# Optimization experiments

Measured on AMD Instinct MI355X. Metric: run time of the kernel, lower is better.

The kernel has to match this reference:

```python
import jax, jax.numpy as jnp
import numpy as np

B, T, C = 4, 4096, 1024
H = 16
D = C // H
EPS = 1e-06


def setup_inputs() -> dict:
    key = jax.random.key(0)
    k1, k2, k3 = jax.random.split(key, 3)
    x = jax.random.normal(k1, (B, T, C), dtype=jnp.float32)
    Wqkv = jax.random.normal(k2, (3 * C, C), dtype=jnp.float32) * (1.0 / np.sqrt(C))
    Wproj = jax.random.normal(k3, (C, C), dtype=jnp.float32) * (1.0 / np.sqrt(C))
    bproj = jnp.zeros((C,), dtype=jnp.float32)
    return {"x": x, "Wqkv": Wqkv, "Wproj": Wproj, "bproj": bproj}


def _phi(x):
    # elu(x) + 1 kernel feature map (non-negative)
    return jax.nn.elu(x) + 1.0


def reference(x, Wqkv, Wproj, bproj):
    b, t, c = x.shape
    qkv = jnp.einsum('btc,ec->bte', x, Wqkv)              # (B,T,3C)
    qkv = qkv.reshape(b, t, 3, H, D)
    q, k, v = qkv[:, :, 0], qkv[:, :, 1], qkv[:, :, 2]     # (B,T,H,D)
    q = _phi(q)
    k = _phi(k)
    # kv state: sum over sequence of outer products k_d v_m -> (B,H,D,D)
    kv = jnp.einsum('bnhd,bnhm->bhdm', k, v)
    k_sum = k.sum(axis=1)                                  # (B,H,D)
    out = jnp.einsum('bnhd,bhdm->bnhm', q, kv)             # (B,T,H,D)
    normalizer = jnp.einsum('bnhd,bhd->bnh', q, k_sum) + EPS
    out = out / normalizer[..., None]
    out = out.reshape(b, t, c)
    out = jnp.einsum('btc,oc->bto', out, Wproj) + bproj
    return out
```

## Files before the change

kernel.cpp:

```cpp
#include <hip/hip_runtime.h>

typedef __bf16 bf16;
typedef bf16 bf16x8 __attribute__((ext_vector_type(8)));
typedef bf16 bf16x4 __attribute__((ext_vector_type(4)));
typedef float f32x4 __attribute__((ext_vector_type(4)));

#define B_ 4
#define T_ 4096
#define C_ 1024
#define EPS_ 1e-6f
#define KVTSTR 16448

typedef __attribute__((address_space(1))) const void* as1p;
typedef __attribute__((address_space(3))) void* as3p;

__global__ void cast_all(const float* __restrict__ x, const float* __restrict__ wq,
                         const float* __restrict__ wp, bf16* __restrict__ xw,
                         bf16* __restrict__ wqw, bf16* __restrict__ wpw) {
  const int N0 = 16777216 / 8, N1 = 3145728 / 8, N2 = 1048576 / 8;
  int i = blockIdx.x * blockDim.x + threadIdx.x;
  const int stride = gridDim.x * blockDim.x;
  for (; i < N0 + N1 + N2; i += stride) {
    const float* src;
    bf16* dst;
    int j;
    if (i < N0) { src = x; dst = xw; j = i; }
    else if (i < N0 + N1) { src = wq; dst = wqw; j = i - N0; }
    else { src = wp; dst = wpw; j = i - N0 - N1; }
    const float4* p = (const float4*)(src + (size_t)j * 8);
    float4 v0 = p[0];
    float4 v1 = p[1];
    bf16x8 o;
    o[0] = (bf16)v0.x; o[1] = (bf16)v0.y; o[2] = (bf16)v0.z; o[3] = (bf16)v0.w;
    o[4] = (bf16)v1.x; o[5] = (bf16)v1.y; o[6] = (bf16)v1.z; o[7] = (bf16)v1.w;
    *(bf16x8*)(dst + (size_t)j * 8) = o;
  }
}

#define BM 256
#define BN 256
#define BK 64
#define KD 1024
#define NTI (KD / BK)
#define TILB 32768
#define BUFB (2 * TILB)
#define SMEMB (2 * BUFB)

#define STG(p, ko, dst) __builtin_amdgcn_global_load_lds((as1p)((p) + (ko)), (as3p)(dst), 16, 0, 0)

#define LDA(MI0)                                                                       \
  _Pragma("unroll") for (int a = 0; a < 2; a++)                                        \
    _Pragma("unroll") for (int kk = 0; kk < 2; kk++)                                   \
      af[a][kk] = *(const bf16x8*)(Ab + (wm * 128 + ((MI0) + a) * 16 + fr) * 64 + swz[kk]);

#define MM(MI0)                                                                        \
  __builtin_amdgcn_s_setprio(1);                                                       \
  _Pragma("unroll") for (int a = 0; a < 2; a++)                                        \
    _Pragma("unroll") for (int nj = 0; nj < 4; nj++)                                   \
      _Pragma("unroll") for (int kk = 0; kk < 2; kk++)                                 \
        acc[(MI0) + a][nj] = __builtin_amdgcn_mfma_f32_16x16x32_bf16(af[a][kk], bfr[nj][kk], acc[(MI0) + a][nj], 0, 0, 0); \
  __builtin_amdgcn_s_setprio(0);

#define BAR1 { __builtin_amdgcn_s_barrier(); asm volatile("s_waitcnt lgkmcnt(0)" ::: "memory"); __builtin_amdgcn_sched_barrier(0); }
#define BAR2 { __builtin_amdgcn_s_barrier(); __builtin_amdgcn_sched_barrier(0); }

template <int MODE>
__global__ __launch_bounds__(512, 1) void gemmX(
    const bf16* __restrict__ A, const bf16* __restrict__ Bm,
    void* __restrict__ Cout, const float* __restrict__ bias,
    bf16* __restrict__ kvt, int M, int N, int tiles_n) {
  extern __shared__ char smem[];
  const int tid = threadIdx.x;
  const int l = tid & 63;
  const int w = tid >> 6;
  const int wm = w >> 2;
  const int wn = w & 3;

  const int cpx = gridDim.x >> 3;
  const int bid = (blockIdx.x & 7) * cpx + (blockIdx.x >> 3);
  const int tm = (bid / tiles_n) * BM;
  const int tn = (bid % tiles_n) * BN;

  const int gsw = ((tid & 7) ^ ((tid >> 3) & 7)) * 8;
  const int tsr = tid >> 3;

  const bf16* pA0 = A + (size_t)(tm + tsr) * KD + gsw;
  const bf16* pA1 = A + (size_t)(tm + 64 + tsr) * KD + gsw;
  const bf16* pA2 = A + (size_t)(tm + 128 + tsr) * KD + gsw;
  const bf16* pA3 = A + (size_t)(tm + 192 + tsr) * KD + gsw;
  const bf16* pB0 = Bm + (size_t)(tn + tsr) * KD + gsw;
  const bf16* pB1 = Bm + (size_t)(tn + 64 + tsr) * KD + gsw;
  const bf16* pB2 = Bm + (size_t)(tn + 128 + tsr) * KD + gsw;
  const bf16* pB3 = Bm + (size_t)(tn + 192 + tsr) * KD + gsw;

  const int fr = l & 15;
  const int fc = l >> 4;
  int swz[2];
  swz[0] = ((0 * 4 + fc) ^ (fr & 7)) * 8;
  swz[1] = ((1 * 4 + fc) ^ (fr & 7)) * 8;

  f32x4 acc[8][4] = {};

  STG(pB0, 0, smem + TILB + tid * 16);
  STG(pB1, 0, smem + TILB + 8192 + tid * 16);
  STG(pB2, 0, smem + TILB + 16384 + tid * 16);
  STG(pB3, 0, smem + TILB + 24576 + tid * 16);
  STG(pA0, 0, smem + tid * 16);
  STG(pA2, 0, smem + 16384 + tid * 16);
  STG(pA1, 0, smem + 8192 + tid * 16);
  STG(pA3, 0, smem + 24576 + tid * 16);
  asm volatile("s_waitcnt vmcnt(2)" ::: "memory");
  __builtin_amdgcn_s_barrier();
  __builtin_amdgcn_sched_barrier(0);

  for (int t = 0; t < NTI; ++t) {
    const bf16* Ab = (const bf16*)(smem + (t & 1) * BUFB);
    const bf16* Bb = (const bf16*)(smem + (t & 1) * BUFB + TILB);
    char* sd = smem + ((t & 1) ^ 1) * BUFB;
    const bool st = (t + 1 < NTI);
    const int ko = (t + 1) * BK;
    bf16x8 bfr[4][2], af[2][2];

#pragma unroll
    for (int nj = 0; nj < 4; nj++)
#pragma unroll
      for (int kk = 0; kk < 2; kk++)
        bfr[nj][kk] = *(const bf16x8*)(Bb + (wn * 64 + nj * 16 + fr) * 64 + swz[kk]);
    LDA(0)
    if (st) {
      STG(pB0, ko, sd + TILB + tid * 16);
      STG(pB1, ko, sd + TILB + 8192 + tid * 16);
      STG(pB2, ko, sd + TILB + 16384 + tid * 16);
      STG(pB3, ko, sd + TILB + 24576 + tid * 16);
    }
    BAR1 MM(0) BAR2

    LDA(2)
    if (st) {
      STG(pA0, ko, sd + tid * 16);
      STG(pA2, ko, sd + 16384 + tid * 16);
      STG(pA1, ko, sd + 8192 + tid * 16);
      STG(pA3, ko, sd + 24576 + tid * 16);
    }
    BAR1 MM(2)
    if (st) { asm volatile("s_waitcnt vmcnt(8)" ::: "memory"); }
    else    { asm volatile("s_waitcnt vmcnt(0)" ::: "memory"); }
    BAR2

    LDA(4)
    BAR1 MM(4) BAR2

    LDA(6)
    BAR1 MM(6)
    if (st) { asm volatile("s_waitcnt vmcnt(2)" ::: "memory"); }
    BAR2
  }

  const int crow0 = tm + wm * 128 + (l >> 4) * 4;
  const int ccol0 = tn + wn * 64 + (l & 15);
  if (MODE == 0) {
    if (tn < 1024) {
      bf16* qbuf = (bf16*)Cout;
#pragma unroll
      for (int mi = 0; mi < 8; mi++)
#pragma unroll
        for (int nj = 0; nj < 4; nj++) {
          const int col = ccol0 + nj * 16;
#pragma unroll
          for (int r = 0; r < 4; r++) {
            const int row = crow0 + mi * 16 + r;
            float v = acc[mi][nj][r];
            v = (v > 0.f) ? (v + 1.0f) : __expf(v);
            qbuf[(size_t)row * 1024 + col] = (bf16)v;
          }
        }
    } else {
#pragma unroll
      for (int mi = 0; mi < 8; mi++)
#pragma unroll
        for (int nj = 0; nj < 4; nj++) {
          const int colp = ccol0 + nj * 16 - 1024;
          const bool isk = (colp < 1024);
          bf16x4 pk;
#pragma unroll
          for (int r = 0; r < 4; r++) {
            float v = acc[mi][nj][r];
            if (isk) v = (v > 0.f) ? (v + 1.0f) : __expf(v);
            pk[r] = (bf16)v;
          }
          const int n0 = crow0 + mi * 16;
          *(bf16x4*)(kvt + (size_t)colp * KVTSTR + n0) = pk;
        }
    }
  } else {
    float* Cf = (float*)Cout;
#pragma unroll
    for (int mi = 0; mi < 8; mi++)
#pragma unroll
      for (int nj = 0; nj < 4; nj++) {
        const int col = ccol0 + nj * 16;
        const float bv = bias[col];
#pragma unroll
        for (int r = 0; r < 4; r++) {
          const int row = crow0 + mi * 16 + r;
          Cf[(size_t)row * N + col] = acc[mi][nj][r] + bv;
        }
      }
  }
}

__global__ __launch_bounds__(256) void kvgemm(const bf16* __restrict__ kvt,
                                              float* __restrict__ partial) {
  const int kc = blockIdx.x >> 6;
  const int bh = blockIdx.x & 63;
  const int b = bh >> 4, h = bh & 15;
  const int l = threadIdx.x & 63;
  const int w = threadIdx.x >> 6;

  const size_t nb = (size_t)b * 4096 + kc * 1024 + (l >> 4) * 8;
  const bf16* Ar = kvt + (size_t)(h * 64 + w * 16 + (l & 15)) * KVTSTR + nb;
  const bf16* Br = kvt + (size_t)(1024 + h * 64 + (l & 15)) * KVTSTR + nb;

  f32x4 acc[4] = {};
  float ks = 0.f;
  bf16x8 aC, bC[4], aN, bN[4];
  aC = *(const bf16x8*)Ar;
#pragma unroll
  for (int nj = 0; nj < 4; nj++) bC[nj] = *(const bf16x8*)(Br + (size_t)nj * 16 * KVTSTR);

  for (int it = 0; it < 32; ++it) {
    if (it + 1 < 32) {
      aN = *(const bf16x8*)(Ar + (it + 1) * 32);
#pragma unroll
      for (int nj = 0; nj < 4; nj++)
        bN[nj] = *(const bf16x8*)(Br + (size_t)nj * 16 * KVTSTR + (it + 1) * 32);
    }
#pragma unroll
    for (int i = 0; i < 8; i++) ks += (float)aC[i];
#pragma unroll
    for (int nj = 0; nj < 4; nj++)
      acc[nj] = __builtin_amdgcn_mfma_f32_16x16x32_bf16(aC, bC[nj], acc[nj], 0, 0, 0);
    aC = aN;
#pragma unroll
    for (int nj = 0; nj < 4; nj++) bC[nj] = bN[nj];
  }

  ks += __shfl_xor(ks, 16);
  ks += __shfl_xor(ks, 32);

  float* p = partial + (size_t)(kc * 64 + bh) * 4160;
#pragma unroll
  for (int nj = 0; nj < 4; nj++) {
    const int m = nj * 16 + (l & 15);
#pragma unroll
    for (int r = 0; r < 4; r++) {
      const int d = w * 16 + (l >> 4) * 4 + r;
      p[d * 64 + m] = acc[nj][r];
    }
  }
  if (l < 16) p[4096 + w * 16 + l] = ks;
}

__global__ void kv_finalize(const float* __restrict__ partial, bf16* __restrict__ kvb) {
  const int bh = blockIdx.x;
  for (int i = threadIdx.x; i < 80 * 64; i += 256) {
    const int row = i >> 6;
    const int dd = i & 63;
    float outv = 0.f;
    if (row < 64) {
      float s = 0.f;
#pragma unroll
      for (int kc = 0; kc < 4; kc++)
        s += partial[(size_t)(kc * 64 + bh) * 4160 + dd * 64 + row];
      outv = s;
    } else if (row < 66) {
      float s = 0.f;
#pragma unroll
      for (int kc = 0; kc < 4; kc++)
        s += partial[(size_t)(kc * 64 + bh) * 4160 + 4096 + dd];
      bf16 hi = (bf16)s;
      outv = (row == 64) ? (float)hi : (s - (float)hi);
    }
    kvb[(size_t)bh * 5120 + row * 64 + dd] = (bf16)outv;
  }
}

__global__ __launch_bounds__(256) void attn_mfma(const bf16* __restrict__ qbuf,
                                                 const bf16* __restrict__ kvb,
                                                 bf16* __restrict__ attn) {
  const int bh = blockIdx.x >> 4;
  const int tch = blockIdx.x & 15;
  const int b = bh >> 4;
  const int h = bh & 15;
  const int lane = threadIdx.x & 63;
  const int wave = threadIdx.x >> 6;
  const int t0 = tch * 256 + wave * 64;

  const bf16* kvp = kvb + (size_t)bh * 5120;
  bf16x8 bfrag[5][2];
#pragma unroll
  for (int j = 0; j < 5; j++)
#pragma unroll
    for (int kk = 0; kk < 2; kk++)
      bfrag[j][kk] = *(const bf16x8*)(kvp + (j * 16 + (lane & 15)) * 64 + kk * 32 + (lane >> 4) * 8);

  f32x4 acc[4][5] = {};
#pragma unroll
  for (int i = 0; i < 4; i++) {
    const int t = t0 + i * 16 + (lane & 15);
    const bf16* qp = qbuf + (size_t)(b * T_ + t) * 1024 + h * 64 + (lane >> 4) * 8;
    bf16x8 a0 = *(const bf16x8*)qp;
    bf16x8 a1 = *(const bf16x8*)(qp + 32);
#pragma unroll
    for (int j = 0; j < 5; j++) {
      acc[i][j] = __builtin_amdgcn_mfma_f32_16x16x32_bf16(a0, bfrag[j][0], acc[i][j], 0, 0, 0);
      acc[i][j] = __builtin_amdgcn_mfma_f32_16x16x32_bf16(a1, bfrag[j][1], acc[i][j], 0, 0, 0);
    }
  }

#pragma unroll
  for (int i = 0; i < 4; i++) {
#pragma unroll
    for (int r = 0; r < 4; r++) {
      float hi = __shfl(acc[i][4][r], (lane & 48));
      float lo = __shfl(acc[i][4][r], (lane & 48) + 1);
      float inv = 1.0f / (hi + lo + EPS_);
      const int t = t0 + i * 16 + (lane >> 4) * 4 + r;
      bf16* op = attn + (size_t)(b * T_ + t) * 1024 + h * 64 + (lane & 15);
#pragma unroll
      for (int j = 0; j < 4; j++)
        op[j * 16] = (bf16)(acc[i][j][r] * inv);
    }
  }
}

extern "C" void kernel_launch(void* const* d_in, const int* in_sizes, int n_in,
                              void* d_out, int out_size, void* d_ws, size_t ws_size,
                              hipStream_t stream) {
  const float* x = (const float*)d_in[0];
  const float* Wqkv = (const float*)d_in[1];
  const float* Wproj = (const float*)d_in[2];
  const float* bproj = (const float*)d_in[3];
  float* out = (float*)d_out;

  char* w = (char*)d_ws;
  bf16* xw = (bf16*)w;      w += (size_t)16777216 * 2;
  bf16* wqkv = (bf16*)w;    w += (size_t)3145728 * 2;
  bf16* wproj = (bf16*)w;   w += (size_t)1048576 * 2;
  bf16* qbuf = (bf16*)w;    w += (size_t)16384 * 1024 * 2;
  bf16* kvt = (bf16*)w;     w += (size_t)2048 * KVTSTR * 2;
  bf16* attnb = (bf16*)w;   w += (size_t)16384 * 1024 * 2;
  float* partial = (float*)w; w += (size_t)4 * 64 * 4160 * 4;
  bf16* kvb = (bf16*)w;

  (void)hipFuncSetAttribute((const void*)gemmX<0>,
      hipFuncAttributeMaxDynamicSharedMemorySize, SMEMB);
  (void)hipFuncSetAttribute((const void*)gemmX<1>,
      hipFuncAttributeMaxDynamicSharedMemorySize, SMEMB);

  cast_all<<<2048, 256, 0, stream>>>(x, Wqkv, Wproj, xw, wqkv, wproj);

  gemmX<0><<<768, 512, SMEMB, stream>>>(xw, wqkv, (void*)qbuf, nullptr, kvt, 16384, 3072, 12);

  kvgemm<<<256, 256, 0, stream>>>(kvt, partial);
  kv_finalize<<<64, 256, 0, stream>>>(partial, kvb);

  attn_mfma<<<64 * 16, 256, 0, stream>>>(qbuf, kvb, attnb);

  gemmX<1><<<256, 512, SMEMB, stream>>>(attnb, wproj, (void*)out, bproj, nullptr, 16384, 1024, 4);
}
```

Before: 221.1 us.

## Replace 256x256 GEMM tiles with 128x256 BK32 tiles and higher occupancy

New measurement: 236.6 us. 1.07x slower.

```diff
diff --git a/kernel.cpp b/kernel.cpp
--- a/kernel.cpp
+++ b/kernel.cpp
@@ -37,39 +37,23 @@
   }
 }
 
-#define BM 256
+#define BM 128
 #define BN 256
-#define BK 64
+#define BK 32
 #define KD 1024
 #define NTI (KD / BK)
-#define TILB 32768
-#define BUFB (2 * TILB)
-#define SMEMB (2 * BUFB)
+#define ABY 8192
+#define BBY 16384
+#define BUFBY (ABY + BBY)
 
 #define STG(p, ko, dst) __builtin_amdgcn_global_load_lds((as1p)((p) + (ko)), (as3p)(dst), 16, 0, 0)
 
-#define LDA(MI0)                                                                       \
-  _Pragma("unroll") for (int a = 0; a < 2; a++)                                        \
-    _Pragma("unroll") for (int kk = 0; kk < 2; kk++)                                   \
-      af[a][kk] = *(const bf16x8*)(Ab + (wm * 128 + ((MI0) + a) * 16 + fr) * 64 + swz[kk]);
-
-#define MM(MI0)                                                                        \
-  __builtin_amdgcn_s_setprio(1);                                                       \
-  _Pragma("unroll") for (int a = 0; a < 2; a++)                                        \
-    _Pragma("unroll") for (int nj = 0; nj < 4; nj++)                                   \
-      _Pragma("unroll") for (int kk = 0; kk < 2; kk++)                                 \
-        acc[(MI0) + a][nj] = __builtin_amdgcn_mfma_f32_16x16x32_bf16(af[a][kk], bfr[nj][kk], acc[(MI0) + a][nj], 0, 0, 0); \
-  __builtin_amdgcn_s_setprio(0);
-
-#define BAR1 { __builtin_amdgcn_s_barrier(); asm volatile("s_waitcnt lgkmcnt(0)" ::: "memory"); __builtin_amdgcn_sched_barrier(0); }
-#define BAR2 { __builtin_amdgcn_s_barrier(); __builtin_amdgcn_sched_barrier(0); }
-
 template <int MODE>
-__global__ __launch_bounds__(512, 1) void gemmX(
+__global__ __launch_bounds__(512, 4) void gemmT(
     const bf16* __restrict__ A, const bf16* __restrict__ Bm,
     void* __restrict__ Cout, const float* __restrict__ bias,
     bf16* __restrict__ kvt, int M, int N, int tiles_n) {
-  extern __shared__ char smem[];
+  __shared__ char smem[2 * BUFBY];
   const int tid = threadIdx.x;
   const int l = tid & 63;
   const int w = tid >> 6;
@@ -81,88 +65,66 @@
   const int tm = (bid / tiles_n) * BM;
   const int tn = (bid % tiles_n) * BN;
 
-  const int gsw = ((tid & 7) ^ ((tid >> 3) & 7)) * 8;
-  const int tsr = tid >> 3;
+  const int gsw = ((tid & 3) ^ ((tid >> 3) & 3)) * 8;
+  const int tsr = tid >> 2;
 
   const bf16* pA0 = A + (size_t)(tm + tsr) * KD + gsw;
-  const bf16* pA1 = A + (size_t)(tm + 64 + tsr) * KD + gsw;
-  const bf16* pA2 = A + (size_t)(tm + 128 + tsr) * KD + gsw;
-  const bf16* pA3 = A + (size_t)(tm + 192 + tsr) * KD + gsw;
   const bf16* pB0 = Bm + (size_t)(tn + tsr) * KD + gsw;
-  const bf16* pB1 = Bm + (size_t)(tn + 64 + tsr) * KD + gsw;
-  const bf16* pB2 = Bm + (size_t)(tn + 128 + tsr) * KD + gsw;
-  const bf16* pB3 = Bm + (size_t)(tn + 192 + tsr) * KD + gsw;
+  const bf16* pB1 = Bm + (size_t)(tn + 128 + tsr) * KD + gsw;
 
   const int fr = l & 15;
   const int fc = l >> 4;
-  int swz[2];
-  swz[0] = ((0 * 4 + fc) ^ (fr & 7)) * 8;
-  swz[1] = ((1 * 4 + fc) ^ (fr & 7)) * 8;
-
-  f32x4 acc[8][4] = {};
-
-  STG(pB0, 0, smem + TILB + tid * 16);
-  STG(pB1, 0, smem + TILB + 8192 + tid * 16);
-  STG(pB2, 0, smem + TILB + 16384 + tid * 16);
-  STG(pB3, 0, smem + TILB + 24576 + tid * 16);
+  const int fsw = (fc ^ ((fr >> 1) & 3)) * 8;
+
+  f32x4 acc[4][4] = {};
+
   STG(pA0, 0, smem + tid * 16);
-  STG(pA2, 0, smem + 16384 + tid * 16);
-  STG(pA1, 0, smem + 8192 + tid * 16);
-  STG(pA3, 0, smem + 24576 + tid * 16);
-  asm volatile("s_waitcnt vmcnt(2)" ::: "memory");
+  STG(pB0, 0, smem + ABY + tid * 16);
+  STG(pB1, 0, smem + ABY + 8192 + tid * 16);
+  asm volatile("s_waitcnt vmcnt(0)" ::: "memory");
   __builtin_amdgcn_s_barrier();
   __builtin_amdgcn_sched_barrier(0);
 
+#pragma unroll 2
   for (int t = 0; t < NTI; ++t) {
-    const bf16* Ab = (const bf16*)(smem + (t & 1) * BUFB);
-    const bf16* Bb = (const bf16*)(smem + (t & 1) * BUFB + TILB);
-    char* sd = smem + ((t & 1) ^ 1) * BUFB;
-    const bool st = (t + 1 < NTI);
-    const int ko = (t + 1) * BK;
-    bf16x8 bfr[4][2], af[2][2];
-
+    char* rb = smem + (t & 1) * BUFBY;
+    char* sd = smem + ((t & 1) ^ 1) * BUFBY;
+    if (t + 1 < NTI) {
+      const int ko = (t + 1) * BK;
+      STG(pA0, ko, sd + tid * 16);
+      STG(pB0, ko, sd + ABY + tid * 16);
+      STG(pB1, ko, sd + ABY + 8192 + tid * 16);
+    }
+    const bf16* Ab = (const bf16*)rb;
+    const bf16* Bb = (const bf16*)(rb + ABY);
+    bf16x8 af[4], bfr[4];
+#pragma unroll
+    for (int mi = 0; mi < 4; mi++)
+      af[mi] = *(const bf16x8*)(Ab + (wm * 64 + mi * 16 + fr) * 32 + fsw);
 #pragma unroll
     for (int nj = 0; nj < 4; nj++)
-#pragma unroll
-      for (int kk = 0; kk < 2; kk++)
-        bfr[nj][kk] = *(const bf16x8*)(Bb + (wn * 64 + nj * 16 + fr) * 64 + swz[kk]);
-    LDA(0)
-    if (st) {
-      STG(pB0, ko, sd + TILB + tid * 16);
-      STG(pB1, ko, sd + TILB + 8192 + tid * 16);
-      STG(pB2, ko, sd + TILB + 16384 + tid * 16);
-      STG(pB3, ko, sd + TILB + 24576 + tid * 16);
-    }
-    BAR1 MM(0) BAR2
-
-    LDA(2)
-    if (st) {
-      STG(pA0, ko, sd + tid * 16);
-      STG(pA2, ko, sd + 16384 + tid * 16);
-      STG(pA1, ko, sd + 8192 + tid * 16);
-      STG(pA3, ko, sd + 24576 + tid * 16);
-    }
-    BAR1 MM(2)
-    if (st) { asm volatile("s_waitcnt vmcnt(8)" ::: "memory"); }
-    else    { asm volatile("s_waitcnt vmcnt(0)" ::: "memory"); }
-    BAR2
-
-    LDA(4)
-    BAR1 MM(4) BAR2
-
-    LDA(6)
-    BAR1 MM(6)
-    if (st) { asm volatile("s_waitcnt vmcnt(2)" ::: "memory"); }
-    BAR2
-  }
-
-  const int crow0 = tm + wm * 128 + (l >> 4) * 4;
+      bfr[nj] = *(const bf16x8*)(Bb + (wn * 64 + nj * 16 + fr) * 32 + fsw);
+    asm volatile("s_waitcnt lgkmcnt(0)" ::: "memory");
+    __builtin_amdgcn_sched_barrier(0);
+    __builtin_amdgcn_s_setprio(1);
+#pragma unroll
+    for (int mi = 0; mi < 4; mi++)
+#pragma unroll
+      for (int nj = 0; nj < 4; nj++)
+        acc[mi][nj] = __builtin_amdgcn_mfma_f32_16x16x32_bf16(af[mi], bfr[nj], acc[mi][nj], 0, 0, 0);
+    __builtin_amdgcn_s_setprio(0);
+    asm volatile("s_waitcnt vmcnt(0)" ::: "memory");
+    __builtin_amdgcn_s_barrier();
+    __builtin_amdgcn_sched_barrier(0);
+  }
+
+  const int crow0 = tm + wm * 64 + (l >> 4) * 4;
   const int ccol0 = tn + wn * 64 + (l & 15);
   if (MODE == 0) {
     if (tn < 1024) {
       bf16* qbuf = (bf16*)Cout;
 #pragma unroll
-      for (int mi = 0; mi < 8; mi++)
+      for (int mi = 0; mi < 4; mi++)
 #pragma unroll
         for (int nj = 0; nj < 4; nj++) {
           const int col = ccol0 + nj * 16;
@@ -176,7 +138,7 @@
         }
     } else {
 #pragma unroll
-      for (int mi = 0; mi < 8; mi++)
+      for (int mi = 0; mi < 4; mi++)
 #pragma unroll
         for (int nj = 0; nj < 4; nj++) {
           const int colp = ccol0 + nj * 16 - 1024;
@@ -195,7 +157,7 @@
   } else {
     float* Cf = (float*)Cout;
 #pragma unroll
-    for (int mi = 0; mi < 8; mi++)
+    for (int mi = 0; mi < 4; mi++)
 #pragma unroll
       for (int nj = 0; nj < 4; nj++) {
         const int col = ccol0 + nj * 16;
@@ -353,19 +315,14 @@
   float* partial = (float*)w; w += (size_t)4 * 64 * 4160 * 4;
   bf16* kvb = (bf16*)w;
 
-  (void)hipFuncSetAttribute((const void*)gemmX<0>,
-      hipFuncAttributeMaxDynamicSharedMemorySize, SMEMB);
-  (void)hipFuncSetAttribute((const void*)gemmX<1>,
-      hipFuncAttributeMaxDynamicSharedMemorySize, SMEMB);
-
   cast_all<<<2048, 256, 0, stream>>>(x, Wqkv, Wproj, xw, wqkv, wproj);
 
-  gemmX<0><<<768, 512, SMEMB, stream>>>(xw, wqkv, (void*)qbuf, nullptr, kvt, 16384, 3072, 12);
+  gemmT<0><<<1536, 512, 0, stream>>>(xw, wqkv, (void*)qbuf, nullptr, kvt, 16384, 3072, 12);
 
   kvgemm<<<256, 256, 0, stream>>>(kvt, partial);
   kv_finalize<<<64, 256, 0, stream>>>(partial, kvb);
 
   attn_mfma<<<64 * 16, 256, 0, stream>>>(qbuf, kvb, attnb);
 
-  gemmX<1><<<256, 512, SMEMB, stream>>>(attnb, wproj, (void*)out, bproj, nullptr, 16384, 1024, 4);
-}
+  gemmT<1><<<512, 512, 0, stream>>>(attnb, wproj, (void*)out, bproj, nullptr, 16384, 1024, 4);
+}
```
